# Performance work log

Measured on AMD Instinct MI355X. Metric: run time of the kernel, lower is better.

Reference implementation:

```python
import jax, jax.numpy as jnp
import numpy as np

B, S, D, H = 2, 2048, 1024, 16
HD = D // H  # head_dim = 64


def setup_inputs() -> dict:
    key = jax.random.key(0)
    ks = jax.random.split(key, 6)
    scale = 0.02
    x = jax.random.normal(ks[0], (B, S, D), dtype=jnp.float32)
    Wq = jax.random.normal(ks[1], (D, D), dtype=jnp.float32) * scale
    Wk = jax.random.normal(ks[2], (D, D), dtype=jnp.float32) * scale
    Wv = jax.random.normal(ks[3], (D, D), dtype=jnp.float32) * scale
    Wo = jax.random.normal(ks[4], (D, D), dtype=jnp.float32) * scale
    bo = jnp.zeros((D,), dtype=jnp.float32)
    return {"x": x, "Wq": Wq, "Wk": Wk, "Wv": Wv, "Wo": Wo, "bo": bo}


def reference(x, Wq, Wk, Wv, Wo, bo):
    b, s, _ = x.shape
    # Linear projections (qkv_bias=False), split into heads: [b, h, s, hd]
    def split_heads(t):
        return t.reshape(b, s, H, HD).transpose(0, 2, 1, 3)
    q = split_heads(x @ Wq)
    k = split_heads(x @ Wk)
    v = split_heads(x @ Wv)
    # Scaled dot-product scores: [b, h, s, s]
    scores = jnp.einsum('bhqd,bhkd->bhqk', q, k) / jnp.sqrt(jnp.float32(HD))
    # Causal mask: triu(ones, diagonal=1) positions -> -inf
    causal = jnp.triu(jnp.ones((s, s), dtype=bool), k=1)
    scores = jnp.where(causal, -jnp.inf, scores)
    attn = jax.nn.softmax(scores, axis=-1)
    # dropout p=0.0 (eval-equivalent): identity
    ctx = jnp.einsum('bhqk,bhkd->bhqd', attn, v)  # [b, h, s, hd]
    ctx = ctx.transpose(0, 2, 1, 3).reshape(b, s, D)
    return ctx @ Wo + bo
```

## Files before the change

kernel.cpp:

```cpp
#include <hip/hip_runtime.h>
#include <math.h>

#define BB 2
#define SS 2048
#define DD 1024
#define HH 16
#define HD 64
#define MM (BB * SS)

typedef __bf16 bf16;
typedef __attribute__((ext_vector_type(8))) __bf16 bf16x8;
typedef __attribute__((ext_vector_type(4))) __bf16 bf16x4;
typedef __attribute__((ext_vector_type(4))) float f32x4;

__device__ __forceinline__ void gld_lds16(const void* g, void* l) {
    __builtin_amdgcn_global_load_lds(
        (const __attribute__((address_space(1))) void*)g,
        (__attribute__((address_space(3))) void*)l, 16, 0, 0);
}

__global__ __launch_bounds__(256) void prep(
    const float* __restrict__ x,
    const float* __restrict__ W0, const float* __restrict__ W1,
    const float* __restrict__ W2, const float* __restrict__ W3,
    bf16* __restrict__ xb, bf16* __restrict__ Wt)
{
    __shared__ float tile[32][33];
    const int z = blockIdx.z;
    if (z < 4) {
        const float* W = (z == 0) ? W0 : (z == 1) ? W1 : (z == 2) ? W2 : W3;
        bf16* O = Wt + (size_t)z * DD * DD;
        const int tx = threadIdx.x & 31, ty = threadIdx.x >> 5;
        const int k0 = blockIdx.y * 32, n0 = blockIdx.x * 32;
#pragma unroll
        for (int i = 0; i < 4; ++i)
            tile[ty + i * 8][tx] = W[(size_t)(k0 + ty + i * 8) * DD + n0 + tx];
        __syncthreads();
#pragma unroll
        for (int i = 0; i < 4; ++i)
            O[(size_t)(n0 + ty + i * 8) * DD + k0 + tx] = (bf16)tile[tx][ty + i * 8];
    } else {
        const int lb = (z - 4) * 1024 + blockIdx.y * 32 + blockIdx.x;
        const size_t i = ((size_t)lb * 256 + threadIdx.x) * 8;
        const float4 a = *(const float4*)(x + i);
        const float4 b = *(const float4*)(x + i + 4);
        bf16x8 o;
        o[0] = (bf16)a.x; o[1] = (bf16)a.y; o[2] = (bf16)a.z; o[3] = (bf16)a.w;
        o[4] = (bf16)b.x; o[5] = (bf16)b.y; o[6] = (bf16)b.z; o[7] = (bf16)b.w;
        *(bf16x8*)(xb + i) = o;
    }
}

template<bool SWAP>
__device__ __forceinline__ void mfma_core(
    const bf16* __restrict__ A, const bf16* __restrict__ Bt,
    int bm, int bn, int K, bf16* As, bf16* Bs, f32x4 (&acc)[4][4])
{
    const int t = threadIdx.x;
    const int w = t >> 6;
    const int l16 = t & 15, quad = (t >> 4) & 3;
    const int wr = w >> 1, wc = w & 1;
    const int r0 = t >> 3;
    const int cs = t & 7;

    for (int k0 = 0; k0 < K; k0 += 64) {
#pragma unroll
        for (int j = 0; j < 4; ++j) {
            const int row = j * 32 + r0;
            const int c = (cs - row) & 7;
            gld_lds16(A  + (size_t)(bm + row) * K + k0 + c * 8,
                      As + (j * 32 + w * 8) * 64);
            gld_lds16(Bt + (size_t)(bn + row) * K + k0 + c * 8,
                      Bs + (j * 32 + w * 8) * 64);
        }
        __syncthreads();

#pragma unroll
        for (int h = 0; h < 2; ++h) {
            bf16x8 af[4], bv[4];
#pragma unroll
            for (int i = 0; i < 4; ++i) {
                const int ra = wr * 64 + i * 16 + l16;
                af[i] = *(const bf16x8*)(As + ra * 64 + (((h * 4 + quad) + ra) & 7) * 8);
                const int rb = wc * 64 + i * 16 + l16;
                bv[i] = *(const bf16x8*)(Bs + rb * 64 + (((h * 4 + quad) + rb) & 7) * 8);
            }
#pragma unroll
            for (int mi = 0; mi < 4; ++mi)
#pragma unroll
                for (int ni = 0; ni < 4; ++ni)
                    acc[mi][ni] = SWAP
                        ? __builtin_amdgcn_mfma_f32_16x16x32_bf16(bv[mi], af[ni], acc[mi][ni], 0, 0, 0)
                        : __builtin_amdgcn_mfma_f32_16x16x32_bf16(af[mi], bv[ni], acc[mi][ni], 0, 0, 0);
        }
        __syncthreads();
    }
}

__global__ __launch_bounds__(256) void gemm_qkv(
    const bf16* __restrict__ xb, const bf16* __restrict__ Wt,
    bf16* __restrict__ Qb, bf16* __restrict__ Kb, bf16* __restrict__ Vb)
{
    __shared__ __align__(16) bf16 As[128 * 64];
    __shared__ __align__(16) bf16 Bs[128 * 64];
    const int bm = blockIdx.y * 128, bn = blockIdx.x * 128, z = blockIdx.z;
    const bf16* Wz = Wt + (size_t)z * DD * DD;

    const int t = threadIdx.x;
    const int w = t >> 6, l16 = t & 15, quad = (t >> 4) & 3;
    const int wr = w >> 1, wc = w & 1;

    f32x4 acc[4][4] = {};
    if (z < 2) {
        mfma_core<true>(xb, Wz, bm, bn, DD, As, Bs, acc);
        bf16* outp = (z == 0) ? Qb : Kb;
#pragma unroll
        for (int mi = 0; mi < 4; ++mi) {
            const int feat = bn + wc * 64 + mi * 16 + quad * 4;
            const int h = feat >> 6, hd = feat & 63;
#pragma unroll
            for (int ni = 0; ni < 4; ++ni) {
                const int tok = bm + wr * 64 + ni * 16 + l16;
                const int b = tok >> 11, s = tok & (SS - 1);
                bf16x4 o;
#pragma unroll
                for (int r = 0; r < 4; ++r) o[r] = (bf16)acc[mi][ni][r];
                *(bf16x4*)(outp + ((size_t)((b * HH + h) * SS + s)) * HD + hd) = o;
            }
        }
    } else {
        mfma_core<false>(xb, Wz, bm, bn, DD, As, Bs, acc);
#pragma unroll
        for (int mi = 0; mi < 4; ++mi) {
            const int tok0 = bm + wr * 64 + mi * 16 + quad * 4;
            const int b = tok0 >> 11, s0 = tok0 & (SS - 1);
#pragma unroll
            for (int ni = 0; ni < 4; ++ni) {
                const int feat = bn + wc * 64 + ni * 16 + l16;
                const int h = feat >> 6, hd = feat & 63;
                bf16x4 o;
#pragma unroll
                for (int r = 0; r < 4; ++r) o[r] = (bf16)acc[mi][ni][r];
                *(bf16x4*)(Vb + ((size_t)((b * HH + h) * HD + hd)) * SS + s0) = o;
            }
        }
    }
}

__global__ __launch_bounds__(256) void gemm_out(
    const bf16* __restrict__ ctx, const bf16* __restrict__ Wto,
    const float* __restrict__ bias, float* __restrict__ out)
{
    __shared__ __align__(16) bf16 As[128 * 64];
    __shared__ __align__(16) bf16 Bs[64 * 64];

    const int L = blockIdx.x;
    const int bm = (L >> 4) * 128;
    const int bn = (L & 15) * 64;

    const int t = threadIdx.x;
    const int w = t >> 6, l16 = t & 15, quad = (t >> 4) & 3;
    const int wr = w >> 1, wc = w & 1;
    const int r0 = t >> 3, cs = t & 7;

    f32x4 acc[2][4] = {};

    for (int k0 = 0; k0 < DD; k0 += 64) {
#pragma unroll
        for (int j = 0; j < 4; ++j) {
            const int row = j * 32 + r0;
            const int c = (cs - row) & 7;
            gld_lds16(ctx + (size_t)(bm + row) * DD + k0 + c * 8,
                      As + (j * 32 + w * 8) * 64);
        }
#pragma unroll
        for (int j = 0; j < 2; ++j) {
            const int row = j * 32 + r0;
            const int c = (cs - row) & 7;
            gld_lds16(Wto + (size_t)(bn + row) * DD + k0 + c * 8,
                      Bs + (j * 32 + w * 8) * 64);
        }
        __syncthreads();

#pragma unroll
        for (int h = 0; h < 2; ++h) {
            bf16x8 af[4], bv[2];
#pragma unroll
            for (int i = 0; i < 4; ++i) {
                const int ra = wr * 64 + i * 16 + l16;
                af[i] = *(const bf16x8*)(As + ra * 64 + (((h * 4 + quad) + ra) & 7) * 8);
            }
#pragma unroll
            for (int i = 0; i < 2; ++i) {
                const int rb = wc * 32 + i * 16 + l16;
                bv[i] = *(const bf16x8*)(Bs + rb * 64 + (((h * 4 + quad) + rb) & 7) * 8);
            }
#pragma unroll
            for (int fi = 0; fi < 2; ++fi)
#pragma unroll
                for (int ti = 0; ti < 4; ++ti)
                    acc[fi][ti] = __builtin_amdgcn_mfma_f32_16x16x32_bf16(
                        bv[fi], af[ti], acc[fi][ti], 0, 0, 0);
        }
        __syncthreads();
    }

#pragma unroll
    for (int fi = 0; fi < 2; ++fi) {
        const int feat = bn + wc * 32 + fi * 16 + quad * 4;
        const float4 bb = *(const float4*)(bias + feat);
#pragma unroll
        for (int ti = 0; ti < 4; ++ti) {
            const int tok = bm + wr * 64 + ti * 16 + l16;
            float4 o;
            o.x = acc[fi][ti][0] + bb.x;
            o.y = acc[fi][ti][1] + bb.y;
            o.z = acc[fi][ti][2] + bb.z;
            o.w = acc[fi][ti][3] + bb.w;
            *(float4*)(out + (size_t)tok * DD + feat) = o;
        }
    }
}

#define PROWS 72
__global__ __launch_bounds__(256) void attn_flash(
    const bf16* __restrict__ Q, const bf16* __restrict__ K,
    const bf16* __restrict__ Vt, bf16* __restrict__ ctx)
{
    __shared__ __align__(16) bf16 Ks[2][64 * 64];
    __shared__ __align__(16) bf16 Vs[2][64 * 64];
    __shared__ __align__(16) bf16 Pl[4][32 * PROWS];

    const int t = threadIdx.x;
    const int w = t >> 6;
    const int lane = t & 63;
    const int l16 = lane & 15, quad = lane >> 4;

    const int L  = blockIdx.x;
    const int bh = L & 31;
    const int qg = 15 - (L >> 5);
    const int q0w = qg * 128 + w * 32;

    const bf16* Qp = Q  + ((size_t)bh * SS + q0w) * HD;
    const bf16* Kp = K  + (size_t)bh * SS * HD;
    const bf16* Vp = Vt + (size_t)bh * HD * SS;
    bf16* Pw = &Pl[w][0];

    bf16x8 bQ[2][2];
#pragma unroll
    for (int qs = 0; qs < 2; ++qs)
#pragma unroll
        for (int c = 0; c < 2; ++c)
            bQ[qs][c] = *(const bf16x8*)(Qp + (qs * 16 + l16) * HD + c * 32 + quad * 8);

    f32x4 accO[4][2] = {};
    float Lr[2] = {0.f, 0.f};
    const float cl2 = 0.125f * 1.44269504f;

    const int r8 = lane >> 3, cs = lane & 7;
    const int nkt = 2 * qg + 2;

#pragma unroll
    for (int j = 0; j < 2; ++j) {
        const int region = w * 2 + j;
        const int row = region * 8 + r8;
        const int c = (cs - row) & 7;
        gld_lds16(Kp + (size_t)row * HD + c * 8, &Ks[0][region * 512]);
        gld_lds16(Vp + (size_t)row * SS + c * 8, &Vs[0][region * 512]);
    }

    for (int kt = 0; kt < nkt; ++kt) {
        const int kb = kt * 64;
        const int buf = kt & 1;
        __syncthreads();

        if (kt + 1 < nkt) {
            const int kb2 = kb + 64;
#pragma unroll
            for (int j = 0; j < 2; ++j) {
                const int region = w * 2 + j;
                const int row = region * 8 + r8;
                const int c = (cs - row) & 7;
                gld_lds16(Kp + (size_t)(kb2 + row) * HD + c * 8, &Ks[buf ^ 1][region * 512]);
                gld_lds16(Vp + (size_t)row * SS + kb2 + c * 8, &Vs[buf ^ 1][region * 512]);
            }
        }

        if (kb <= q0w + 31) {
            const bf16* Kbuf = &Ks[buf][0];
            const bf16* Vbuf = &Vs[buf][0];

            f32x4 St[4][2] = {};
#pragma unroll
            for (int mi = 0; mi < 4; ++mi) {
                const int row = mi * 16 + l16;
                const bf16x8 a0 = *(const bf16x8*)(Kbuf + row * 64 + ((quad + row) & 7) * 8);
                const bf16x8 a1 = *(const bf16x8*)(Kbuf + row * 64 + ((quad + 4 + row) & 7) * 8);
#pragma unroll
                for (int qs = 0; qs < 2; ++qs) {
                    St[mi][qs] = __builtin_amdgcn_mfma_f32_16x16x32_bf16(a0, bQ[qs][0], St[mi][qs], 0, 0, 0);
                    St[mi][qs] = __builtin_amdgcn_mfma_f32_16x16x32_bf16(a1, bQ[qs][1], St[mi][qs], 0, 0, 0);
                }
            }

            if (kb + 63 > q0w) {
#pragma unroll
                for (int qs = 0; qs < 2; ++qs) {
                    const int qrow = q0w + qs * 16 + l16;
#pragma unroll
                    for (int mi = 0; mi < 4; ++mi)
#pragma unroll
                        for (int r = 0; r < 4; ++r)
                            if (kb + mi * 16 + quad * 4 + r > qrow) St[mi][qs][r] = -1e30f;
                }
            }

#pragma unroll
            for (int qs = 0; qs < 2; ++qs) {
                float rs = 0.f;
#pragma unroll
                for (int mi = 0; mi < 4; ++mi) {
                    bf16x4 pk;
#pragma unroll
                    for (int r = 0; r < 4; ++r) {
                        const float p = exp2f(St[mi][qs][r] * cl2);
                        rs += p;
                        pk[r] = (bf16)p;
                    }
                    *(bf16x4*)(Pw + (qs * 16 + l16) * PROWS + mi * 16 + quad * 4) = pk;
                }
                rs += __shfl_xor(rs, 16);
                rs += __shfl_xor(rs, 32);
                Lr[qs] += rs;
            }

#pragma unroll
            for (int kc = 0; kc < 2; ++kc) {
                bf16x8 bP[2];
#pragma unroll
                for (int qs = 0; qs < 2; ++qs)
                    bP[qs] = *(const bf16x8*)(Pw + (qs * 16 + l16) * PROWS + kc * 32 + quad * 8);
#pragma unroll
                for (int mi = 0; mi < 4; ++mi) {
                    const int row = mi * 16 + l16;
                    const bf16x8 aV = *(const bf16x8*)(
                        Vbuf + row * 64 + (((kc * 4 + quad) + row) & 7) * 8);
#pragma unroll
                    for (int qs = 0; qs < 2; ++qs)
                        accO[mi][qs] = __builtin_amdgcn_mfma_f32_16x16x32_bf16(
                            aV, bP[qs], accO[mi][qs], 0, 0, 0);
                }
            }
        }
    }

    const int b = bh >> 4, h = bh & (HH - 1);
#pragma unroll
    for (int qs = 0; qs < 2; ++qs) {
        const float rinv = 1.0f / Lr[qs];
        bf16* op = ctx + ((size_t)(b * SS + q0w + qs * 16 + l16)) * DD + h * HD;
#pragma unroll
        for (int mi = 0; mi < 4; ++mi) {
            bf16x4 o;
#pragma unroll
            for (int r = 0; r < 4; ++r) o[r] = (bf16)(accO[mi][qs][r] * rinv);
            *(bf16x4*)(op + mi * 16 + quad * 4) = o;
        }
    }
}

extern "C" void kernel_launch(void* const* d_in, const int* in_sizes, int n_in,
                              void* d_out, int out_size, void* d_ws, size_t ws_size,
                              hipStream_t stream)
{
    const float* x  = (const float*)d_in[0];
    const float* Wq = (const float*)d_in[1];
    const float* Wk = (const float*)d_in[2];
    const float* Wv = (const float*)d_in[3];
    const float* Wo = (const float*)d_in[4];
    const float* bo = (const float*)d_in[5];
    float* out = (float*)d_out;

    const size_t chunk = (size_t)MM * DD;
    bf16* xb  = (bf16*)d_ws;
    bf16* Wt  = xb + chunk;
    bf16* Qb  = Wt + 4 * (size_t)DD * DD;
    bf16* Kb  = Qb + chunk;
    bf16* Vb  = Kb + chunk;
    bf16* ctx = Vb + chunk;

    prep<<<dim3(32, 32, 6), dim3(256), 0, stream>>>(x, Wq, Wk, Wv, Wo, xb, Wt);

    gemm_qkv<<<dim3(DD / 128, MM / 128, 3), dim3(256), 0, stream>>>(xb, Wt, Qb, Kb, Vb);

    attn_flash<<<dim3(512), dim3(256), 0, stream>>>(Qb, Kb, Vb, ctx);

    gemm_out<<<dim3(512), dim3(256), 0, stream>>>(
        ctx, Wt + 3 * (size_t)DD * DD, bo, out);
}
```

Baseline: 206.1 us.

## Pair high and low causal query tiles per block to balance attention work

Each attention block now handles two 64-row query groups, one from the end and one from the start of the sequence. Every warp owns 16 rows of each group instead of 32 contiguous rows, so all blocks do roughly equal causal work. Beyond the low group's diagonal only one query slice is computed through a templated tile function. The goal is to remove load imbalance and wasted warp work from causal masking. In exchange, each K/V tile is reused across fewer query rows per warp, and the code carries two template instantiations.

```diff
diff --git a/kernel.cpp b/kernel.cpp
--- a/kernel.cpp
+++ b/kernel.cpp
@@ -223,6 +223,75 @@
 }
 
 #define PROWS 72
+template<int NG>
+__device__ __forceinline__ void attn_tile(
+    const bf16* __restrict__ Kbuf, const bf16* __restrict__ Vbuf,
+    bf16* __restrict__ Pw, const bf16x8 (&bQ)[2][2], const int (&qbase)[2],
+    int kb, int l16, int quad, f32x4 (&accO)[4][2], float (&Lr)[2], float cl2)
+{
+    f32x4 St[4][NG] = {};
+#pragma unroll
+    for (int mi = 0; mi < 4; ++mi) {
+        const int row = mi * 16 + l16;
+        const bf16x8 a0 = *(const bf16x8*)(Kbuf + row * 64 + ((quad + row) & 7) * 8);
+        const bf16x8 a1 = *(const bf16x8*)(Kbuf + row * 64 + ((quad + 4 + row) & 7) * 8);
+#pragma unroll
+        for (int qs = 0; qs < NG; ++qs) {
+            St[mi][qs] = __builtin_amdgcn_mfma_f32_16x16x32_bf16(a0, bQ[qs][0], St[mi][qs], 0, 0, 0);
+            St[mi][qs] = __builtin_amdgcn_mfma_f32_16x16x32_bf16(a1, bQ[qs][1], St[mi][qs], 0, 0, 0);
+        }
+    }
+
+#pragma unroll
+    for (int qs = 0; qs < NG; ++qs) {
+        if (kb + 63 > qbase[qs]) {
+            const int qrow = qbase[qs] + l16;
+#pragma unroll
+            for (int mi = 0; mi < 4; ++mi)
+#pragma unroll
+                for (int r = 0; r < 4; ++r)
+                    if (kb + mi * 16 + quad * 4 + r > qrow) St[mi][qs][r] = -1e30f;
+        }
+    }
+
+#pragma unroll
+    for (int qs = 0; qs < NG; ++qs) {
+        float rs = 0.f;
+#pragma unroll
+        for (int mi = 0; mi < 4; ++mi) {
+            bf16x4 pk;
+#pragma unroll
+            for (int r = 0; r < 4; ++r) {
+                const float p = exp2f(St[mi][qs][r] * cl2);
+                rs += p;
+                pk[r] = (bf16)p;
+            }
+            *(bf16x4*)(Pw + (qs * 16 + l16) * PROWS + mi * 16 + quad * 4) = pk;
+        }
+        rs += __shfl_xor(rs, 16);
+        rs += __shfl_xor(rs, 32);
+        Lr[qs] += rs;
+    }
+
+#pragma unroll
+    for (int kc = 0; kc < 2; ++kc) {
+        bf16x8 bP[NG];
+#pragma unroll
+        for (int qs = 0; qs < NG; ++qs)
+            bP[qs] = *(const bf16x8*)(Pw + (qs * 16 + l16) * PROWS + kc * 32 + quad * 8);
+#pragma unroll
+        for (int mi = 0; mi < 4; ++mi) {
+            const int row = mi * 16 + l16;
+            const bf16x8 aV = *(const bf16x8*)(
+                Vbuf + row * 64 + (((kc * 4 + quad) + row) & 7) * 8);
+#pragma unroll
+            for (int qs = 0; qs < NG; ++qs)
+                accO[mi][qs] = __builtin_amdgcn_mfma_f32_16x16x32_bf16(
+                    aV, bP[qs], accO[mi][qs], 0, 0, 0);
+        }
+    }
+}
+
 __global__ __launch_bounds__(256) void attn_flash(
     const bf16* __restrict__ Q, const bf16* __restrict__ K,
     const bf16* __restrict__ Vt, bf16* __restrict__ ctx)
@@ -238,10 +307,14 @@
 
     const int L  = blockIdx.x;
     const int bh = L & 31;
-    const int qg = 15 - (L >> 5);
-    const int q0w = qg * 128 + w * 32;
-
-    const bf16* Qp = Q  + ((size_t)bh * SS + q0w) * HD;
+    const int pr = L >> 5;
+    const int gh = 31 - pr;
+    const int gl = pr;
+    int qbase[2];
+    qbase[0] = gh * 64 + w * 16;
+    qbase[1] = gl * 64 + w * 16;
+
+    const bf16* Qp = Q  + (size_t)bh * SS * HD;
     const bf16* Kp = K  + (size_t)bh * SS * HD;
     const bf16* Vp = Vt + (size_t)bh * HD * SS;
     bf16* Pw = &Pl[w][0];
@@ -251,14 +324,14 @@
     for (int qs = 0; qs < 2; ++qs)
 #pragma unroll
         for (int c = 0; c < 2; ++c)
-            bQ[qs][c] = *(const bf16x8*)(Qp + (qs * 16 + l16) * HD + c * 32 + quad * 8);
+            bQ[qs][c] = *(const bf16x8*)(Qp + (size_t)(qbase[qs] + l16) * HD + c * 32 + quad * 8);
 
     f32x4 accO[4][2] = {};
     float Lr[2] = {0.f, 0.f};
     const float cl2 = 0.125f * 1.44269504f;
 
     const int r8 = lane >> 3, cs = lane & 7;
-    const int nkt = 2 * qg + 2;
+    const int nkt = gh + 1;
 
 #pragma unroll
     for (int j = 0; j < 2; ++j) {
@@ -286,79 +359,19 @@
             }
         }
 
-        if (kb <= q0w + 31) {
-            const bf16* Kbuf = &Ks[buf][0];
-            const bf16* Vbuf = &Vs[buf][0];
-
-            f32x4 St[4][2] = {};
-#pragma unroll
-            for (int mi = 0; mi < 4; ++mi) {
-                const int row = mi * 16 + l16;
-                const bf16x8 a0 = *(const bf16x8*)(Kbuf + row * 64 + ((quad + row) & 7) * 8);
-                const bf16x8 a1 = *(const bf16x8*)(Kbuf + row * 64 + ((quad + 4 + row) & 7) * 8);
-#pragma unroll
-                for (int qs = 0; qs < 2; ++qs) {
-                    St[mi][qs] = __builtin_amdgcn_mfma_f32_16x16x32_bf16(a0, bQ[qs][0], St[mi][qs], 0, 0, 0);
-                    St[mi][qs] = __builtin_amdgcn_mfma_f32_16x16x32_bf16(a1, bQ[qs][1], St[mi][qs], 0, 0, 0);
-                }
-            }
-
-            if (kb + 63 > q0w) {
-#pragma unroll
-                for (int qs = 0; qs < 2; ++qs) {
-                    const int qrow = q0w + qs * 16 + l16;
-#pragma unroll
-                    for (int mi = 0; mi < 4; ++mi)
-#pragma unroll
-                        for (int r = 0; r < 4; ++r)
-                            if (kb + mi * 16 + quad * 4 + r > qrow) St[mi][qs][r] = -1e30f;
-                }
-            }
-
-#pragma unroll
-            for (int qs = 0; qs < 2; ++qs) {
-                float rs = 0.f;
-#pragma unroll
-                for (int mi = 0; mi < 4; ++mi) {
-                    bf16x4 pk;
-#pragma unroll
-                    for (int r = 0; r < 4; ++r) {
-                        const float p = exp2f(St[mi][qs][r] * cl2);
-                        rs += p;
-                        pk[r] = (bf16)p;
-                    }
-                    *(bf16x4*)(Pw + (qs * 16 + l16) * PROWS + mi * 16 + quad * 4) = pk;
-                }
-                rs += __shfl_xor(rs, 16);
-                rs += __shfl_xor(rs, 32);
-                Lr[qs] += rs;
-            }
-
-#pragma unroll
-            for (int kc = 0; kc < 2; ++kc) {
-                bf16x8 bP[2];
-#pragma unroll
-                for (int qs = 0; qs < 2; ++qs)
-                    bP[qs] = *(const bf16x8*)(Pw + (qs * 16 + l16) * PROWS + kc * 32 + quad * 8);
-#pragma unroll
-                for (int mi = 0; mi < 4; ++mi) {
-                    const int row = mi * 16 + l16;
-                    const bf16x8 aV = *(const bf16x8*)(
-                        Vbuf + row * 64 + (((kc * 4 + quad) + row) & 7) * 8);
-#pragma unroll
-                    for (int qs = 0; qs < 2; ++qs)
-                        accO[mi][qs] = __builtin_amdgcn_mfma_f32_16x16x32_bf16(
-                            aV, bP[qs], accO[mi][qs], 0, 0, 0);
-                }
-            }
-        }
+        if (kt <= gl)
+            attn_tile<2>(&Ks[buf][0], &Vs[buf][0], Pw, bQ, qbase, kb,
+                         l16, quad, accO, Lr, cl2);
+        else
+            attn_tile<1>(&Ks[buf][0], &Vs[buf][0], Pw, bQ, qbase, kb,
+                         l16, quad, accO, Lr, cl2);
     }
 
     const int b = bh >> 4, h = bh & (HH - 1);
 #pragma unroll
     for (int qs = 0; qs < 2; ++qs) {
         const float rinv = 1.0f / Lr[qs];
-        bf16* op = ctx + ((size_t)(b * SS + q0w + qs * 16 + l16)) * DD + h * HD;
+        bf16* op = ctx + ((size_t)(b * SS + qbase[qs] + l16)) * DD + h * HD;
 #pragma unroll
         for (int mi = 0; mi < 4; ++mi) {
             bf16x4 o;
```

After: 196.4 us. 1.05x faster.
